# Performance work log

Measured on AMD Instinct MI355X. Metric: run time of the kernel, lower is better.

The kernel has to match this reference:

```python
import jax, jax.numpy as jnp
import numpy as np
from functools import partial

T, B, CH, H, W = 16, 4, 128, 128, 128
TAU, VTH, ALPHA, EPS = 2.0, 1.0, 2.0, 1e-5

# ATan surrogate-gradient spike (spikingjelly surrogate.ATan, alpha=2.0)
@jax.custom_vjp
def spike(x):
    return (x >= 0.0).astype(x.dtype)

def _spike_fwd(x):
    return spike(x), x

def _spike_bwd(x, g):
    return (g * (ALPHA / 2.0) / (1.0 + (jnp.pi / 2.0 * ALPHA * x) ** 2),)

spike.defvjp(_spike_fwd, _spike_bwd)

def _conv(x, w):  # x [N,C,H,W], w [O,I,3,3], padding=1 -> SAME
    return jax.lax.conv_general_dilated(x, w, (1, 1), 'SAME',
                                        dimension_numbers=('NCHW', 'OIHW', 'NCHW'))

def _bn(x, g, b, m, v):  # inference-mode BatchNorm2d, channel axis 1
    inv = g / jnp.sqrt(v + EPS)
    return x * inv[:, None, None] + (b - m * inv)[:, None, None]

def _pool(x):  # MaxPool2d(2,2), NCHW
    return jax.lax.reduce_window(x, -jnp.inf, jax.lax.max,
                                 (1, 1, 2, 2), (1, 1, 2, 2), 'VALID')

def _lif(xs):  # xs [T, ...]; LIFNode: tau=2, v_th=1, v_reset=0, decay_input, hard reset (detached)
    def step(v, x):
        v = v + (x - v) / TAU                      # charge
        s = spike(v - VTH)                         # fire (Heaviside fwd, ATan bwd)
        v = v * (1.0 - jax.lax.stop_gradient(s))   # detached hard reset to 0
        return v, s
    return jax.lax.scan(step, jnp.zeros_like(xs[0]), xs)[1]

def _block(xs, w, g, b, m, v):  # conv -> BN -> LIF -> maxpool, xs [T,B,C,H,W]
    t, bs = xs.shape[0], xs.shape[1]
    y = _bn(_conv(xs.reshape((t * bs,) + xs.shape[2:]), w), g, b, m, v)
    y = _lif(y.reshape((t, bs) + y.shape[1:]))
    y = _pool(y.reshape((t * bs,) + y.shape[2:]))
    return y.reshape((t, bs) + y.shape[1:])


def setup_inputs() -> dict:
    key = jax.random.key(0)
    ks = jax.random.split(key, 8)
    inp = {'x': jax.random.uniform(ks[0], (T, B, 2, H, W), jnp.float32)}
    fan_ins = [2 * 9, CH * 9, CH * 9, CH * 9]
    for i in range(4):
        cin = 2 if i == 0 else CH
        inp[f'w{i+1}'] = jax.random.normal(ks[i + 1], (CH, cin, 3, 3), jnp.float32) * np.sqrt(2.0 / fan_ins[i]).astype(np.float32)
        inp[f'g{i+1}'] = jnp.ones((CH,), jnp.float32)
        inp[f'b{i+1}'] = jnp.zeros((CH,), jnp.float32)
        inp[f'm{i+1}'] = jnp.zeros((CH,), jnp.float32)
        inp[f'v{i+1}'] = jnp.ones((CH,), jnp.float32)
    inp['wfc'] = jax.random.normal(ks[5], (10, CH * 8 * 8), jnp.float32) * np.sqrt(1.0 / (CH * 64)).astype(np.float32)
    inp['bfc'] = jnp.zeros((10,), jnp.float32)
    return inp


def reference(x, w1, g1, b1, m1, v1, w2, g2, b2, m2, v2,
              w3, g3, b3, m3, v3, w4, g4, b4, m4, v4, wfc, bfc):
    y = _block(x, w1, g1, b1, m1, v1)   # [T,B,CH,64,64]
    y = _block(y, w2, g2, b2, m2, v2)   # [T,B,CH,32,32]
    y = _block(y, w3, g3, b3, m3, v3)   # [T,B,CH,16,16]
    y = _block(y, w4, g4, b4, m4, v4)   # [T,B,CH,8,8]
    z = y.reshape(y.shape[0], y.shape[1], -1) @ wfc.T + bfc  # [T,B,10]
    return _lif(z)                       # output spike train [T,B,10]
```

## Files before the change

kernel.cpp:

```cpp
#include <hip/hip_runtime.h>
#include <hip/hip_bf16.h>
#include <math.h>

#define T_STEPS 16

typedef __attribute__((ext_vector_type(8))) short bf16x8;
typedef __attribute__((ext_vector_type(16))) float f32x16;

__global__ __launch_bounds__(256) void prep_w_kernel(const float* __restrict__ w,
                                                     __hip_bfloat16* __restrict__ wp) {
  int idx = blockIdx.x * 256 + threadIdx.x;
  if (idx >= 147456) return;
  int co = idx / 1152, rem = idx - co * 1152;
  int ci = rem / 9, tap = rem - ci * 9;
  float x = w[idx];
  float h = (float)__float2bfloat16(x);
  float r1 = x - h;
  float m = (float)__float2bfloat16(r1);
  float r2 = r1 - m;
  size_t base = (((size_t)tap * 16 + (ci >> 3)) * 128 + co) * 8 + (ci & 7);
  const size_t SSZ = 147456;
  wp[base] = __float2bfloat16(h);
  wp[SSZ + base] = __float2bfloat16(m);
  wp[2 * SSZ + base] = __float2bfloat16(r2);
}

__global__ __launch_bounds__(256) void layer1_kernel(
    const float* __restrict__ x, const float* __restrict__ w,
    const float* __restrict__ gn, const float* __restrict__ bn,
    const float* __restrict__ mn, const float* __restrict__ vn,
    __hip_bfloat16* __restrict__ out) {
  const int tid = threadIdx.x;
  const int tile = blockIdx.x;
  const int ty0 = (tile >> 2) * 32, tx0 = (tile & 3) * 32;
  const int co0 = blockIdx.y * 4;
  const int b = blockIdx.z;
  const int qx2 = (tid & 15) * 2;
  const int qy2 = (tid >> 4) * 2;

  float wreg[2][9][4];
#pragma unroll
  for (int j = 0; j < 4; ++j)
#pragma unroll
    for (int ci = 0; ci < 2; ++ci)
#pragma unroll
      for (int tap = 0; tap < 9; ++tap)
        wreg[ci][tap][j] = w[(co0 + j) * 18 + ci * 9 + tap];

  float scale[4], shift[4];
#pragma unroll
  for (int j = 0; j < 4; ++j) {
    float inv = gn[co0 + j] / sqrtf(vn[co0 + j] + 1e-5f);
    scale[j] = inv;
    shift[j] = bn[co0 + j] - mn[co0 + j] * inv;
  }

  float vm[4][4];
#pragma unroll
  for (int j = 0; j < 4; ++j)
#pragma unroll
    for (int p = 0; p < 4; ++p) vm[j][p] = 0.f;

  __shared__ float Il[2 * 34 * 44];

  for (int t = 0; t < T_STEPS; ++t) {
    __syncthreads();
    const float* xt = x + (size_t)((t * 4 + b) * 2) * 16384;
#pragma unroll
    for (int k = 0; k < 3; ++k) {
      int job = k * 256 + tid;
      if (job < 680) {
        int ci = job >= 340 ? 1 : 0;
        int r = job - ci * 340;
        int y = (r * 6554) >> 16;
        int slot = r - y * 10;
        int gy = ty0 - 1 + y;
        int gxb = tx0 - 4 + slot * 4;
        float4 v = make_float4(0.f, 0.f, 0.f, 0.f);
        if ((unsigned)gy < 128u && (unsigned)gxb < 128u)
          v = *(const float4*)(xt + ci * 16384 + gy * 128 + gxb);
        *(float4*)(&Il[ci * 1496 + y * 44 + slot * 4]) = v;
      }
    }
    __syncthreads();

    float acc[4][4];
#pragma unroll
    for (int j = 0; j < 4; ++j)
#pragma unroll
      for (int p = 0; p < 4; ++p) acc[j][p] = 0.f;

#pragma unroll
    for (int ci = 0; ci < 2; ++ci) {
      float iv[4][4];
#pragma unroll
      for (int r = 0; r < 4; ++r) {
        const float* rp = &Il[ci * 1496 + (qy2 + r) * 44 + qx2 + 2];
        float2 pA = *(const float2*)(rp);
        float2 pB = *(const float2*)(rp + 2);
        float2 pC = *(const float2*)(rp + 4);
        iv[r][0] = pA.y; iv[r][1] = pB.x; iv[r][2] = pB.y; iv[r][3] = pC.x;
      }
#pragma unroll
      for (int tap = 0; tap < 9; ++tap) {
        const int dy = tap / 3, dx = tap - dy * 3;
#pragma unroll
        for (int sy = 0; sy < 2; ++sy)
#pragma unroll
          for (int sx = 0; sx < 2; ++sx) {
            float xin = iv[sy + dy][sx + dx];
            acc[0][sy * 2 + sx] += wreg[ci][tap][0] * xin;
            acc[1][sy * 2 + sx] += wreg[ci][tap][1] * xin;
            acc[2][sy * 2 + sx] += wreg[ci][tap][2] * xin;
            acc[3][sy * 2 + sx] += wreg[ci][tap][3] * xin;
          }
      }
    }

    const int py = (ty0 >> 1) + (tid >> 4);
    const int px = (tx0 >> 1) + (tid & 15);
    short4 pk;
    short* pks = (short*)&pk;
#pragma unroll
    for (int j = 0; j < 4; ++j) {
      float pooled = 0.f;
#pragma unroll
      for (int p = 0; p < 4; ++p) {
        float yv = acc[j][p] * scale[j] + shift[j];
        float nv = vm[j][p] + (yv - vm[j][p]) * 0.5f;
        float s = (nv >= 1.0f) ? 1.0f : 0.0f;
        pooled = fmaxf(pooled, s);
        vm[j][p] = (nv >= 1.0f) ? 0.f : nv;
      }
      __hip_bfloat16 bv = __float2bfloat16(pooled);
      pks[j] = *(short*)&bv;
    }
    *(short4*)(out + (((size_t)(t * 4 + b) * 64 + py) * 64 + px) * 128 + co0) = pk;
  }
}

template <int S>
__global__ __launch_bounds__(256) void conv32_kernel(
    const __hip_bfloat16* __restrict__ spk, const __hip_bfloat16* __restrict__ wp,
    float* __restrict__ pre, int t_base) {
  constexpr int TILES_X = S / 8;
  const int tile = blockIdx.x;
  const int ty0 = (tile / TILES_X) * 16;
  const int tx0 = (tile % TILES_X) * 8;
  const int tbl = blockIdx.z;
  const int tbg = t_base * 4 + tbl;
  const int tid = threadIdx.x;
  const int lane = tid & 63;
  const int wv = tid >> 6;

  __shared__ uint4 At4[2880];

  const __hip_bfloat16* sp = spk + (size_t)tbg * S * S * 128;
#pragma unroll
  for (int k = 0; k < 12; ++k) {
    int job = k * 256 + tid;
    if (job < 2880) {
      int c8 = job & 15, r = job >> 4;
      int y = (r * 6554) >> 16;
      int xx = r - y * 10;
      int gy = ty0 - 1 + y, gx = tx0 - 1 + xx;
      uint4 v = make_uint4(0u, 0u, 0u, 0u);
      if ((unsigned)gy < (unsigned)S && (unsigned)gx < (unsigned)S)
        v = *(const uint4*)(sp + ((size_t)(gy * S + gx)) * 128 + c8 * 8);
      At4[(y * 10 + xx) * 16 + (c8 ^ (xx & 7))] = v;
    }
  }
  __syncthreads();

  const int l31 = lane & 31, hh = lane >> 5;
  const int co = wv * 32 + l31;
  const int ly = l31 >> 3, lx = lane & 7;

  f32x16 acc[4];
#pragma unroll
  for (int m = 0; m < 4; ++m)
#pragma unroll
    for (int r = 0; r < 16; ++r) acc[m][r] = 0.f;

  const short* wpb = (const short*)wp + (size_t)co * 8;

  for (int tap = 0; tap < 9; ++tap) {
    const int dy = tap / 3, dx = tap - dy * 3;
    const int xx = lx + dx;
    const int sx7 = xx & 7;
#pragma unroll
    for (int kk = 0; kk < 8; ++kk) {
      const int kc = kk * 2 + hh;
      bf16x8 a[4];
#pragma unroll
      for (int m = 0; m < 4; ++m)
        a[m] = *(const bf16x8*)(At4 + ((m * 4 + ly + dy) * 10 + xx) * 16 + (kc ^ sx7));
#pragma unroll
      for (int s = 0; s < 3; ++s) {
        bf16x8 bfr = *(const bf16x8*)(wpb + ((size_t)(s * 9 + tap) * 16 + kc) * 1024);
#pragma unroll
        for (int m = 0; m < 4; ++m)
          acc[m] = __builtin_amdgcn_mfma_f32_32x32x16_bf16(a[m], bfr, acc[m], 0, 0, 0);
      }
    }
  }

  float* po = pre + (size_t)tbl * S * S * 128 + co;
#pragma unroll
  for (int m = 0; m < 4; ++m)
#pragma unroll
    for (int r = 0; r < 16; ++r) {
      int row = (r & 3) + 8 * (r >> 2) + 4 * hh;
      int p = m * 32 + row;
      po[((size_t)(ty0 + (p >> 3)) * S + tx0 + (p & 7)) * 128] = acc[m][r];
    }
}

template <int S>
__global__ __launch_bounds__(256) void lif_pool_kernel(
    const float* __restrict__ pre, __hip_bfloat16* __restrict__ spk,
    float* __restrict__ vm, const float* __restrict__ gn,
    const float* __restrict__ bn, const float* __restrict__ mn,
    const float* __restrict__ vn, int t_base, int nt) {
  constexpr int OS = S / 2, NQ = OS * OS;
  const int tid = threadIdx.x;
  const int co = tid & 127;
  const int q = blockIdx.x * 2 + (tid >> 7);
  const int b = blockIdx.z;
  const int qy = q / OS, qx = q - qy * OS;
  float inv = gn[co] / sqrtf(vn[co] + 1e-5f);
  float sc = inv, sh = bn[co] - mn[co] * inv;
  float* vp = vm + (((size_t)b * NQ + q) * 4) * 128 + co;
  float v0, v1, v2, v3;
  if (t_base == 0) {
    v0 = v1 = v2 = v3 = 0.f;
  } else {
    v0 = vp[0]; v1 = vp[128]; v2 = vp[256]; v3 = vp[384];
  }
  const size_t rowstride = (size_t)S * 128;
  for (int t = 0; t < nt; ++t) {
    const float* p = pre + (((size_t)(t * 4 + b) * S + qy * 2) * S + qx * 2) * 128 + co;
    float x00 = p[0] * sc + sh;
    float x01 = p[128] * sc + sh;
    float x10 = p[rowstride] * sc + sh;
    float x11 = p[rowstride + 128] * sc + sh;
    float n0 = v0 + (x00 - v0) * 0.5f; float s0 = n0 >= 1.f ? 1.f : 0.f; v0 = n0 >= 1.f ? 0.f : n0;
    float n1 = v1 + (x01 - v1) * 0.5f; float s1 = n1 >= 1.f ? 1.f : 0.f; v1 = n1 >= 1.f ? 0.f : n1;
    float n2 = v2 + (x10 - v2) * 0.5f; float s2 = n2 >= 1.f ? 1.f : 0.f; v2 = n2 >= 1.f ? 0.f : n2;
    float n3 = v3 + (x11 - v3) * 0.5f; float s3 = n3 >= 1.f ? 1.f : 0.f; v3 = n3 >= 1.f ? 0.f : n3;
    float pooled = fmaxf(fmaxf(s0, s1), fmaxf(s2, s3));
    spk[((size_t)((t_base + t) * 4 + b) * NQ + q) * 128 + co] = __float2bfloat16(pooled);
  }
  if (t_base + nt < T_STEPS) {
    vp[0] = v0; vp[128] = v1; vp[256] = v2; vp[384] = v3;
  }
}

__global__ __launch_bounds__(256) void fc_kernel(const __hip_bfloat16* __restrict__ a4,
                                                 const float* __restrict__ wfc,
                                                 const float* __restrict__ bfc,
                                                 float* __restrict__ z) {
  const int tb = blockIdx.x;
  const int tid = threadIdx.x;
  const __hip_bfloat16* a = a4 + (size_t)tb * 8192;
  float part[10];
#pragma unroll
  for (int o = 0; o < 10; ++o) part[o] = 0.f;
  for (int i = tid; i < 8192; i += 256) {
    int co = i >> 6, yx = i & 63;
    float av = __bfloat162float(a[yx * 128 + co]);
#pragma unroll
    for (int o = 0; o < 10; ++o) part[o] += av * wfc[o * 8192 + i];
  }
#pragma unroll
  for (int o = 0; o < 10; ++o)
    for (int off = 32; off > 0; off >>= 1) part[o] += __shfl_xor(part[o], off, 64);
  __shared__ float red[4][10];
  if ((tid & 63) == 0) {
#pragma unroll
    for (int o = 0; o < 10; ++o) red[tid >> 6][o] = part[o];
  }
  __syncthreads();
  if (tid < 10)
    z[tb * 10 + tid] = red[0][tid] + red[1][tid] + red[2][tid] + red[3][tid] + bfc[tid];
}

__global__ void out_lif_kernel(const float* __restrict__ z, float* __restrict__ out) {
  int i = threadIdx.x;
  if (i < 40) {
    float v = 0.f;
    for (int t = 0; t < T_STEPS; ++t) {
      float yv = z[t * 40 + i];
      float nv = v + (yv - v) * 0.5f;
      float s = (nv >= 1.0f) ? 1.0f : 0.0f;
      out[t * 40 + i] = s;
      v = (nv >= 1.0f) ? 0.f : nv;
    }
  }
}

extern "C" void kernel_launch(void* const* d_in, const int* in_sizes, int n_in,
                              void* d_out, int out_size, void* d_ws, size_t ws_size,
                              hipStream_t stream) {
  const float* x = (const float*)d_in[0];
  const float* w1 = (const float*)d_in[1];
  const float* g1 = (const float*)d_in[2];
  const float* b1 = (const float*)d_in[3];
  const float* m1 = (const float*)d_in[4];
  const float* v1 = (const float*)d_in[5];
  const float* w2 = (const float*)d_in[6];
  const float* g2 = (const float*)d_in[7];
  const float* b2 = (const float*)d_in[8];
  const float* m2 = (const float*)d_in[9];
  const float* v2 = (const float*)d_in[10];
  const float* w3 = (const float*)d_in[11];
  const float* g3 = (const float*)d_in[12];
  const float* b3 = (const float*)d_in[13];
  const float* m3 = (const float*)d_in[14];
  const float* v3 = (const float*)d_in[15];
  const float* w4 = (const float*)d_in[16];
  const float* g4 = (const float*)d_in[17];
  const float* b4 = (const float*)d_in[18];
  const float* m4 = (const float*)d_in[19];
  const float* v4 = (const float*)d_in[20];
  const float* wfc = (const float*)d_in[21];
  const float* bfc = (const float*)d_in[22];
  float* out = (float*)d_out;

  float* p = (float*)d_ws;
  __hip_bfloat16* wp2 = (__hip_bfloat16*)p; p += 221184;
  __hip_bfloat16* wp3 = (__hip_bfloat16*)p; p += 221184;
  __hip_bfloat16* wp4 = (__hip_bfloat16*)p; p += 221184;
  __hip_bfloat16* spk1 = (__hip_bfloat16*)p; p += 16777216;
  float* preH = p; p += 16777216;
  __hip_bfloat16* spk2 = (__hip_bfloat16*)p; p += 4194304;
  float* vm2 = p; p += 2097152;
  __hip_bfloat16* spk3 = (__hip_bfloat16*)p; p += 1048576;
  float* vm3 = p; p += 524288;
  __hip_bfloat16* spk4 = (__hip_bfloat16*)p; p += 262144;
  float* vm4 = p; p += 131072;
  float* z = p; p += 640;

  prep_w_kernel<<<576, 256, 0, stream>>>(w2, wp2);
  prep_w_kernel<<<576, 256, 0, stream>>>(w3, wp3);
  prep_w_kernel<<<576, 256, 0, stream>>>(w4, wp4);

  layer1_kernel<<<dim3(16, 32, 4), 256, 0, stream>>>(x, w1, g1, b1, m1, v1, spk1);

  conv32_kernel<64><<<dim3(32, 1, 32), 256, 0, stream>>>(spk1, wp2, preH, 0);
  lif_pool_kernel<64><<<dim3(512, 1, 4), 256, 0, stream>>>(preH, spk2, vm2, g2, b2, m2, v2, 0, 8);
  conv32_kernel<64><<<dim3(32, 1, 32), 256, 0, stream>>>(spk1, wp2, preH, 8);
  lif_pool_kernel<64><<<dim3(512, 1, 4), 256, 0, stream>>>(preH, spk2, vm2, g2, b2, m2, v2, 8, 8);

  conv32_kernel<32><<<dim3(8, 1, 64), 256, 0, stream>>>(spk2, wp3, preH, 0);
  lif_pool_kernel<32><<<dim3(128, 1, 4), 256, 0, stream>>>(preH, spk3, vm3, g3, b3, m3, v3, 0, 16);

  conv32_kernel<16><<<dim3(2, 1, 64), 256, 0, stream>>>(spk3, wp4, preH, 0);
  lif_pool_kernel<16><<<dim3(32, 1, 4), 256, 0, stream>>>(preH, spk4, vm4, g4, b4, m4, v4, 0, 16);

  fc_kernel<<<64, 256, 0, stream>>>(spk4, wfc, bfc, z);
  out_lif_kernel<<<1, 64, 0, stream>>>(z, out);
}
```

Measured before the change: 471.5 us.

## Fuse layer-2 conv with BN/LIF/pool and pre-pad layer-1 input

Layer 2 now runs as a single kernel that keeps each membrane potential in registers across all 16 timesteps and does BN, LIF and 2x2 max-pool in the MFMA epilogue. This removes the fp32 pre-activation round trip through global memory and the separate LIF/pool launches. Layer 1 now reads a zero-padded copy of the input directly into registers, dropping its shared-memory staging and barriers at the cost of an extra pad kernel. The trade-off is that layer 2 has only 512 blocks, each looping serially over time, so parallelism per launch is lower.

```diff
diff --git a/kernel.cpp b/kernel.cpp
--- a/kernel.cpp
+++ b/kernel.cpp
@@ -25,8 +25,22 @@
   wp[2 * SSZ + base] = __float2bfloat16(r2);
 }
 
+__global__ __launch_bounds__(192) void pad_x_kernel(const float* __restrict__ x,
+                                                    float* __restrict__ xp) {
+  const int plane = blockIdx.x;
+  const int row = blockIdx.y;
+  const int c = threadIdx.x;
+  if (c < 132) {
+    float v = 0.f;
+    int gr = row - 1, gc = c - 1;
+    if ((unsigned)gr < 128u && (unsigned)gc < 128u)
+      v = x[(size_t)plane * 16384 + gr * 128 + gc];
+    xp[((size_t)plane * 130 + row) * 132 + c] = v;
+  }
+}
+
 __global__ __launch_bounds__(256) void layer1_kernel(
-    const float* __restrict__ x, const float* __restrict__ w,
+    const float* __restrict__ xp, const float* __restrict__ w,
     const float* __restrict__ gn, const float* __restrict__ bn,
     const float* __restrict__ mn, const float* __restrict__ vn,
     __hip_bfloat16* __restrict__ out) {
@@ -37,6 +51,8 @@
   const int b = blockIdx.z;
   const int qx2 = (tid & 15) * 2;
   const int qy2 = (tid >> 4) * 2;
+  const int yq = ty0 + qy2;
+  const int xq = tx0 + qx2;
 
   float wreg[2][9][4];
 #pragma unroll
@@ -61,28 +77,15 @@
 #pragma unroll
     for (int p = 0; p < 4; ++p) vm[j][p] = 0.f;
 
-  __shared__ float Il[2 * 34 * 44];
-
   for (int t = 0; t < T_STEPS; ++t) {
-    __syncthreads();
-    const float* xt = x + (size_t)((t * 4 + b) * 2) * 16384;
-#pragma unroll
-    for (int k = 0; k < 3; ++k) {
-      int job = k * 256 + tid;
-      if (job < 680) {
-        int ci = job >= 340 ? 1 : 0;
-        int r = job - ci * 340;
-        int y = (r * 6554) >> 16;
-        int slot = r - y * 10;
-        int gy = ty0 - 1 + y;
-        int gxb = tx0 - 4 + slot * 4;
-        float4 v = make_float4(0.f, 0.f, 0.f, 0.f);
-        if ((unsigned)gy < 128u && (unsigned)gxb < 128u)
-          v = *(const float4*)(xt + ci * 16384 + gy * 128 + gxb);
-        *(float4*)(&Il[ci * 1496 + y * 44 + slot * 4]) = v;
-      }
-    }
-    __syncthreads();
+    const float* xpt = xp + (size_t)((t * 4 + b) * 2) * 17160;
+    float iv[2][4][4];
+#pragma unroll
+    for (int ci = 0; ci < 2; ++ci)
+#pragma unroll
+      for (int r = 0; r < 4; ++r)
+        *(float4*)&iv[ci][r][0] =
+            *(const float4*)(xpt + (size_t)(ci * 130 + yq + r) * 132 + xq);
 
     float acc[4][4];
 #pragma unroll
@@ -91,16 +94,7 @@
       for (int p = 0; p < 4; ++p) acc[j][p] = 0.f;
 
 #pragma unroll
-    for (int ci = 0; ci < 2; ++ci) {
-      float iv[4][4];
-#pragma unroll
-      for (int r = 0; r < 4; ++r) {
-        const float* rp = &Il[ci * 1496 + (qy2 + r) * 44 + qx2 + 2];
-        float2 pA = *(const float2*)(rp);
-        float2 pB = *(const float2*)(rp + 2);
-        float2 pC = *(const float2*)(rp + 4);
-        iv[r][0] = pA.y; iv[r][1] = pB.x; iv[r][2] = pB.y; iv[r][3] = pC.x;
-      }
+    for (int ci = 0; ci < 2; ++ci)
 #pragma unroll
       for (int tap = 0; tap < 9; ++tap) {
         const int dy = tap / 3, dx = tap - dy * 3;
@@ -108,14 +102,13 @@
         for (int sy = 0; sy < 2; ++sy)
 #pragma unroll
           for (int sx = 0; sx < 2; ++sx) {
-            float xin = iv[sy + dy][sx + dx];
+            float xin = iv[ci][sy + dy][sx + dx];
             acc[0][sy * 2 + sx] += wreg[ci][tap][0] * xin;
             acc[1][sy * 2 + sx] += wreg[ci][tap][1] * xin;
             acc[2][sy * 2 + sx] += wreg[ci][tap][2] * xin;
             acc[3][sy * 2 + sx] += wreg[ci][tap][3] * xin;
           }
       }
-    }
 
     const int py = (ty0 >> 1) + (tid >> 4);
     const int px = (tx0 >> 1) + (tid & 15);
@@ -123,19 +116,112 @@
     short* pks = (short*)&pk;
 #pragma unroll
     for (int j = 0; j < 4; ++j) {
-      float pooled = 0.f;
+      float mx = -1e30f;
 #pragma unroll
       for (int p = 0; p < 4; ++p) {
         float yv = acc[j][p] * scale[j] + shift[j];
         float nv = vm[j][p] + (yv - vm[j][p]) * 0.5f;
-        float s = (nv >= 1.0f) ? 1.0f : 0.0f;
-        pooled = fmaxf(pooled, s);
+        mx = fmaxf(mx, nv);
         vm[j][p] = (nv >= 1.0f) ? 0.f : nv;
       }
-      __hip_bfloat16 bv = __float2bfloat16(pooled);
+      __hip_bfloat16 bv = __float2bfloat16(mx >= 1.0f ? 1.0f : 0.0f);
       pks[j] = *(short*)&bv;
     }
     *(short4*)(out + (((size_t)(t * 4 + b) * 64 + py) * 64 + px) * 128 + co0) = pk;
+  }
+}
+
+template <int S, int TY, int TX, int NW>
+__global__ __launch_bounds__(NW * 64) void conv_fused2_kernel(
+    const __hip_bfloat16* __restrict__ spk, const __hip_bfloat16* __restrict__ wp,
+    const float* __restrict__ gn, const float* __restrict__ bn,
+    const float* __restrict__ mn, const float* __restrict__ vn,
+    __hip_bfloat16* __restrict__ out) {
+  constexpr int HX = TX + 2;
+  constexpr int NSLOT = (TY + 2) * HX;
+  constexpr int NJOBS = NSLOT * 16;
+  constexpr int NTHR = NW * 64;
+  constexpr int TILES_X = S / TX;
+  constexpr int FR = 32 / TX;
+  constexpr int OS = S / 2;
+
+  const int tile = blockIdx.x;
+  const int ty0 = (tile / TILES_X) * TY;
+  const int tx0 = (tile % TILES_X) * TX;
+  const int cob = blockIdx.y * 32;
+  const int b = blockIdx.z;
+  const int tid = threadIdx.x;
+  const int lane = tid & 63;
+  const int wid = tid >> 6;
+  const int l31 = lane & 31, hh = lane >> 5;
+  const int co = cob + l31;
+  const int pxx = l31 & (TX - 1);
+  const int pyf = l31 / TX;
+
+  __shared__ uint4 At4[NSLOT * 16];
+
+  float sc = gn[co] / sqrtf(vn[co] + 1e-5f);
+  float sh = bn[co] - mn[co] * sc;
+  const short* wb = (const short*)wp + co * 8;
+
+  f32x16 vm;
+#pragma unroll
+  for (int r = 0; r < 16; ++r) vm[r] = 0.f;
+
+  for (int t = 0; t < T_STEPS; ++t) {
+    __syncthreads();
+    const short* spt = (const short*)(spk + (size_t)(t * 4 + b) * S * S * 128);
+    for (int job = tid; job < NJOBS; job += NTHR) {
+      int c8 = job & 15, si = job >> 4;
+      int y = (si * 6554) >> 16;
+      int xx = si - y * 10;
+      int gy = ty0 - 1 + y, gx = tx0 - 1 + xx;
+      uint4 v = make_uint4(0u, 0u, 0u, 0u);
+      if ((unsigned)gy < (unsigned)S && (unsigned)gx < (unsigned)S)
+        v = *(const uint4*)(spt + (gy * S + gx) * 128 + c8 * 8);
+      At4[si * 16 + (c8 ^ (xx & 7))] = v;
+    }
+    __syncthreads();
+
+    f32x16 acc;
+#pragma unroll
+    for (int r = 0; r < 16; ++r) acc[r] = 0.f;
+
+    for (int tap = 0; tap < 9; ++tap) {
+      const int dy = tap / 3, dx = tap - dy * 3;
+      const int xx = pxx + dx;
+      const int srow = (wid * FR + pyf + dy) * HX + xx;
+      const int sx7 = xx & 7;
+#pragma unroll
+      for (int kk = 0; kk < 8; ++kk) {
+        const int kc = kk * 2 + hh;
+        bf16x8 a = *(const bf16x8*)(At4 + srow * 16 + (kc ^ sx7));
+#pragma unroll
+        for (int s = 0; s < 3; ++s) {
+          bf16x8 bfr = *(const bf16x8*)(wb + ((size_t)(s * 9 + tap) * 16 + kc) * 1024);
+          acc = __builtin_amdgcn_mfma_f32_32x32x16_bf16(a, bfr, acc, 0, 0, 0);
+        }
+      }
+    }
+
+    float pooled[4] = {0.f, 0.f, 0.f, 0.f};
+#pragma unroll
+    for (int r = 0; r < 16; ++r) {
+      const int row0 = (r & 3) + 8 * (r >> 2);
+      float yv = acc[r] * sc + sh;
+      float nv = vm[r] + (yv - vm[r]) * 0.5f;
+      int slot = ((row0 >> 3) >> 1) * 2 + ((row0 & 7) >> 1);
+      pooled[slot] = fmaxf(pooled[slot], nv);
+      vm[r] = (nv >= 1.0f) ? 0.f : nv;
+    }
+    __hip_bfloat16* ob = out + (size_t)(t * 4 + b) * OS * OS * 128 + co;
+#pragma unroll
+    for (int q = 0; q < 4; ++q) {
+      int pyg = ((ty0 + wid * 4) >> 1) + (q >> 1);
+      int pxg = (tx0 >> 1) + (q & 1) + 2 * hh;
+      ob[((size_t)pyg * OS + pxg) * 128] =
+          __float2bfloat16(pooled[q] >= 1.0f ? 1.0f : 0.0f);
+    }
   }
 }
 
@@ -331,10 +417,10 @@
   __hip_bfloat16* wp2 = (__hip_bfloat16*)p; p += 221184;
   __hip_bfloat16* wp3 = (__hip_bfloat16*)p; p += 221184;
   __hip_bfloat16* wp4 = (__hip_bfloat16*)p; p += 221184;
+  float* xp = p; p += 2196480;
   __hip_bfloat16* spk1 = (__hip_bfloat16*)p; p += 16777216;
-  float* preH = p; p += 16777216;
   __hip_bfloat16* spk2 = (__hip_bfloat16*)p; p += 4194304;
-  float* vm2 = p; p += 2097152;
+  float* preH = p; p += 8388608;
   __hip_bfloat16* spk3 = (__hip_bfloat16*)p; p += 1048576;
   float* vm3 = p; p += 524288;
   __hip_bfloat16* spk4 = (__hip_bfloat16*)p; p += 262144;
@@ -344,13 +430,12 @@
   prep_w_kernel<<<576, 256, 0, stream>>>(w2, wp2);
   prep_w_kernel<<<576, 256, 0, stream>>>(w3, wp3);
   prep_w_kernel<<<576, 256, 0, stream>>>(w4, wp4);
-
-  layer1_kernel<<<dim3(16, 32, 4), 256, 0, stream>>>(x, w1, g1, b1, m1, v1, spk1);
-
-  conv32_kernel<64><<<dim3(32, 1, 32), 256, 0, stream>>>(spk1, wp2, preH, 0);
-  lif_pool_kernel<64><<<dim3(512, 1, 4), 256, 0, stream>>>(preH, spk2, vm2, g2, b2, m2, v2, 0, 8);
-  conv32_kernel<64><<<dim3(32, 1, 32), 256, 0, stream>>>(spk1, wp2, preH, 8);
-  lif_pool_kernel<64><<<dim3(512, 1, 4), 256, 0, stream>>>(preH, spk2, vm2, g2, b2, m2, v2, 8, 8);
+  pad_x_kernel<<<dim3(128, 130), 192, 0, stream>>>(x, xp);
+
+  layer1_kernel<<<dim3(16, 32, 4), 256, 0, stream>>>(xp, w1, g1, b1, m1, v1, spk1);
+
+  conv_fused2_kernel<64, 16, 8, 4>
+      <<<dim3(32, 4, 4), 256, 0, stream>>>(spk1, wp2, g2, b2, m2, v2, spk2);
 
   conv32_kernel<32><<<dim3(8, 1, 64), 256, 0, stream>>>(spk2, wp3, preH, 0);
   lif_pool_kernel<32><<<dim3(128, 1, 4), 256, 0, stream>>>(preH, spk3, vm3, g3, b3, m3, v3, 0, 16);
```

New measurement: 1.795 ms. 3.81x slower.
